# Kernel tuning notes

Measured on AMD Instinct MI355X. Metric: run time of the kernel, lower is better.

Reference implementation:

```python
import jax, jax.numpy as jnp
from jax import lax
import numpy as np

D_MODEL = 6      # problemDim
ED = 48          # d_inner = expand_factor * d_model = hidden_size
N = 32           # d_state
DCONV = 16       # d_conv
NLAYERS = 2
DT_RANK = 1      # ceil(d_model / 16)
NCLS = 4
B, L = 16, 1024
EPS = 1e-5


def setup_inputs() -> dict:
    key = jax.random.key(0)
    ks = jax.random.split(key, 12)
    rn = lambda k, s, sc=0.1: (jax.random.normal(k, s, dtype=jnp.float32) * sc)
    return {
        "x": jax.random.normal(ks[0], (B, L, D_MODEL), dtype=jnp.float32),
        "in_proj_w": rn(ks[1], (NLAYERS, D_MODEL, 2 * ED)),
        "conv_w": rn(ks[2], (NLAYERS, ED, DCONV)),
        "conv_b": jnp.zeros((NLAYERS, ED), jnp.float32),
        "x_proj_w": rn(ks[3], (NLAYERS, ED, DT_RANK + 2 * N)),
        "dt_w": rn(ks[4], (NLAYERS, DT_RANK, ED), 1.0),
        "dt_b": rn(ks[5], (NLAYERS, ED), 0.5),
        # S4D-real init: A = -[1..N]
        "A_log": jnp.log(jnp.broadcast_to(jnp.arange(1, N + 1, dtype=jnp.float32), (NLAYERS, ED, N))),
        "D": jnp.ones((NLAYERS, ED), jnp.float32),
        "norm_w": jnp.ones((NLAYERS, D_MODEL), jnp.float32),
        "out_proj_w": rn(ks[6], (NLAYERS - 1, ED, D_MODEL)),
        "fc_w": rn(ks[7], (ED, ED)),
        "fc_b": jnp.zeros((ED,), jnp.float32),
        "cls_w": rn(ks[8], (ED, NCLS)),
        "cls_b": jnp.zeros((NCLS,), jnp.float32),
        "reg_w": rn(ks[9], (ED, 1)),
        "reg_b": jnp.zeros((1,), jnp.float32),
    }


def rmsnorm(h, w):
    return h * lax.rsqrt(jnp.mean(h * h, axis=-1, keepdims=True) + EPS) * w


def dwconv_causal(xs, w, b):
    # xs: (B,L,ED), w: (ED,DCONV), b: (ED,) -> causal depthwise conv, output length L
    u = jnp.pad(xs.transpose(0, 2, 1), ((0, 0), (0, 0), (DCONV - 1, 0)))  # (B,ED,L+DCONV-1)
    out = lax.conv_general_dilated(u, w[:, None, :], window_strides=(1,), padding="VALID",
                                   feature_group_count=ED,
                                   dimension_numbers=("NCH", "OIH", "NCH"))  # (B,ED,L)
    return (out + b[None, :, None]).transpose(0, 2, 1)


def selective_scan(deltaA, deltaBx, Cm):
    # deltaA, deltaBx: (B,L,ED,N); Cm: (B,L,N) -> y: (B,L,ED)
    dA = deltaA.transpose(1, 0, 2, 3)
    dBx = deltaBx.transpose(1, 0, 2, 3)
    Ct = Cm.transpose(1, 0, 2)

    def step(h, inp):
        dA_t, dBx_t, C_t = inp
        h = dA_t * h + dBx_t                       # (B,ED,N)
        y = jnp.einsum("ben,bn->be", h, C_t)       # (B,ED)
        return h, y

    h0 = jnp.zeros(dA.shape[1:], dA.dtype)
    _, ys = lax.scan(step, h0, (dA, dBx, Ct))
    return ys.transpose(1, 0, 2)


def mamba_forward(x, in_proj_w, conv_w, conv_b, x_proj_w, dt_w, dt_b, A_log, D,
                  norm_w, out_proj_w, fc_w, fc_b, cls_w, cls_b, reg_w, reg_b):
    h = x
    for i in range(NLAYERS):
        res = h
        u = rmsnorm(h, norm_w[i])
        xz = u @ in_proj_w[i]                      # (B,L,2*ED)
        xs, z = jnp.split(xz, 2, axis=-1)
        xs = jax.nn.silu(dwconv_causal(xs, conv_w[i], conv_b[i]))
        dbc = xs @ x_proj_w[i]                     # (B,L,DT_RANK+2N)
        dlt = dbc[..., :DT_RANK]
        Bm = dbc[..., DT_RANK:DT_RANK + N]
        Cm = dbc[..., DT_RANK + N:]
        delta = jax.nn.softplus(dlt @ dt_w[i] + dt_b[i])   # (B,L,ED)
        A = -jnp.exp(A_log[i])                     # (ED,N)
        deltaA = jnp.exp(delta[..., None] * A)     # (B,L,ED,N)
        deltaBx = delta[..., None] * Bm[:, :, None, :] * xs[..., None]
        y = selective_scan(deltaA, deltaBx, Cm) + D[i] * xs
        y = y * jax.nn.silu(z)
        if i < NLAYERS - 1:
            h = y @ out_proj_w[i] + res
        else:
            h = y  # classifer=True: last block exposes d_inner (=hidden_size) features
    feat = jax.nn.relu(h[:, -1, :] @ fc_w + fc_b)  # (B,ED)
    class_logits = feat @ cls_w + cls_b            # (B,NCLS)
    mass_pred = (feat @ reg_w + reg_b)[..., 0]     # (B,)
    return class_logits, mass_pred


def reference(x, in_proj_w, conv_w, conv_b, x_proj_w, dt_w, dt_b, A_log, D,
              norm_w, out_proj_w, fc_w, fc_b, cls_w, cls_b, reg_w, reg_b):
    return mamba_forward(x, in_proj_w, conv_w, conv_b, x_proj_w, dt_w, dt_b, A_log, D,
                         norm_w, out_proj_w, fc_w, fc_b, cls_w, cls_b, reg_w, reg_b)
```

## Files before the change

### kernel.cpp

```cpp
#include <hip/hip_runtime.h>
#include <math.h>

#define BB 16
#define LL 1024
#define DM 6
#define ED 48
#define NST 32
#define DCONVK 16
#define NCLS 4
#define CH 32
#define HALO 15
#define NCF 16
#define CSF 64

__device__ __forceinline__ float softplus_f(float x) {
    return fmaxf(x, 0.f) + log1pf(expf(-fabsf(x)));
}
__device__ __forceinline__ float silu_f(float x) {
    return x / (1.f + __expf(-x));
}

template<int MODE>
__global__ __launch_bounds__(256) void pre_kernel(
    const float* __restrict__ hin,
    const float* __restrict__ ygT_in,
    const float* __restrict__ opw,
    const float* __restrict__ ipw,
    const float* __restrict__ nw,
    const float* __restrict__ cw,
    const float* __restrict__ cb,
    const float* __restrict__ xpw,
    const float* __restrict__ dtw,
    const float* __restrict__ dtb,
    float* __restrict__ xT,
    float* __restrict__ zT,
    float* __restrict__ dT,
    float* __restrict__ Bi,
    float* __restrict__ Ci)
{
    __shared__ float s_ipw[6*96];
    __shared__ float s_nw[6];
    __shared__ float s_cw[48*DCONVK];
    __shared__ float s_cb[48];
    __shared__ float s_xpw[48*65];
    __shared__ float s_dtw[48];
    __shared__ float s_dtb[48];
    __shared__ float s_opw[48*6];
    __shared__ float s_pp[(CH+HALO)*4*6];
    __shared__ float s_u[(CH+HALO)*7];
    __shared__ float s_raw[(CH+HALO)*49];
    __shared__ float s_xsT[48*CH];
    __shared__ float s_bc[64*33];
    __shared__ float s_dlt[CH];

    const int tid = threadIdx.x;
    const int b  = blockIdx.x >> 5;
    const int l0 = (blockIdx.x & 31) * CH;
    const int ROWS = CH + HALO;

    for (int i = tid; i < 6*96; i += 256) s_ipw[i] = ipw[i];
    if (tid < 6) s_nw[tid] = nw[tid];
    for (int i = tid; i < 48*DCONVK; i += 256) s_cw[i] = cw[i];
    if (tid < 48) s_cb[tid] = cb[tid];
    for (int i = tid; i < 48*65; i += 256) s_xpw[i] = xpw[i];
    if (tid < 48) { s_dtw[tid] = dtw[tid]; s_dtb[tid] = dtb[tid]; }
    if (MODE == 1) for (int i = tid; i < 48*6; i += 256) s_opw[i] = opw[i];
    __syncthreads();

    if (MODE == 0) {
        if (tid < ROWS) {
            int l = l0 - HALO + tid;
            float u[DM];
            if (l >= 0) {
                float ss = 0.f;
                const float* hp = hin + ((size_t)b*LL + l)*DM;
                #pragma unroll
                for (int d = 0; d < DM; ++d) { u[d] = hp[d]; ss += u[d]*u[d]; }
                float sc = rsqrtf(ss * (1.f/DM) + 1e-5f);
                #pragma unroll
                for (int d = 0; d < DM; ++d) u[d] *= sc * s_nw[d];
            } else {
                #pragma unroll
                for (int d = 0; d < DM; ++d) u[d] = 0.f;
            }
            #pragma unroll
            for (int d = 0; d < DM; ++d) s_u[tid*7+d] = u[d];
        }
        __syncthreads();
    } else {
        const int g = tid >> 6, t = tid & 63;
        if (t < ROWS) {
            int l = l0 - HALO + t;
            float pacc[DM] = {0,0,0,0,0,0};
            if (l >= 0) {
                for (int e = g*12; e < g*12 + 12; ++e) {
                    float v = ygT_in[((size_t)b*48 + e)*LL + l];
                    #pragma unroll
                    for (int d = 0; d < DM; ++d) pacc[d] += v * s_opw[e*DM+d];
                }
            }
            #pragma unroll
            for (int d = 0; d < DM; ++d) s_pp[(t*4+g)*DM+d] = pacc[d];
        }
        __syncthreads();
        if (tid < ROWS) {
            int l = l0 - HALO + tid;
            float u[DM];
            if (l >= 0) {
                const float* xr = hin + ((size_t)b*LL + l)*DM;
                float ss = 0.f;
                #pragma unroll
                for (int d = 0; d < DM; ++d) {
                    float hv = s_pp[(tid*4+0)*DM+d] + s_pp[(tid*4+1)*DM+d]
                             + s_pp[(tid*4+2)*DM+d] + s_pp[(tid*4+3)*DM+d] + xr[d];
                    u[d] = hv; ss += hv*hv;
                }
                float sc = rsqrtf(ss * (1.f/DM) + 1e-5f);
                #pragma unroll
                for (int d = 0; d < DM; ++d) u[d] *= sc * s_nw[d];
            } else {
                #pragma unroll
                for (int d = 0; d < DM; ++d) u[d] = 0.f;
            }
            #pragma unroll
            for (int d = 0; d < DM; ++d) s_u[tid*7+d] = u[d];
        }
        __syncthreads();
    }

    for (int i = tid; i < 96*ROWS; i += 256) {
        int j = i / ROWS, t = i - j*ROWS;
        float acc = 0.f;
        #pragma unroll
        for (int d = 0; d < DM; ++d) acc += s_u[t*7+d]*s_ipw[d*96+j];
        if (j < 48) s_raw[t*49+j] = acc;
        else if (t >= HALO)
            zT[((size_t)b*48 + (j-48))*LL + (l0 - HALO + t)] = silu_f(acc);
    }
    __syncthreads();

    for (int o = tid; o < 48*CH; o += 256) {
        int c = o >> 5, p = o & 31;
        float acc = s_cb[c];
        #pragma unroll
        for (int k = 0; k < DCONVK; ++k)
            acc += s_raw[(p+k)*49 + c] * s_cw[c*DCONVK + k];
        float v = silu_f(acc);
        s_xsT[c*CH + p] = v;
        xT[((size_t)b*48 + c)*LL + l0 + p] = v;
    }
    __syncthreads();

    {
        const int j = tid >> 3, g = tid & 7;
        float a0=0,a1=0,a2=0,a3=0;
        float c0=0,c1=0,c2=0,c3=0;
        for (int e = 0; e < 48; ++e) {
            float4 xv = *(const float4*)&s_xsT[e*CH + 4*g];
            float w1 = s_xpw[e*65 + 1 + j];
            float w2 = s_xpw[e*65 + 33 + j];
            a0 = fmaf(xv.x, w1, a0); a1 = fmaf(xv.y, w1, a1);
            a2 = fmaf(xv.z, w1, a2); a3 = fmaf(xv.w, w1, a3);
            c0 = fmaf(xv.x, w2, c0); c1 = fmaf(xv.y, w2, c1);
            c2 = fmaf(xv.z, w2, c2); c3 = fmaf(xv.w, w2, c3);
        }
        s_bc[j*33 + 4*g+0] = a0; s_bc[j*33 + 4*g+1] = a1;
        s_bc[j*33 + 4*g+2] = a2; s_bc[j*33 + 4*g+3] = a3;
        s_bc[(32+j)*33 + 4*g+0] = c0; s_bc[(32+j)*33 + 4*g+1] = c1;
        s_bc[(32+j)*33 + 4*g+2] = c2; s_bc[(32+j)*33 + 4*g+3] = c3;
    }
    if (tid < 32) {
        float acc = 0.f;
        for (int e = 0; e < 48; ++e) acc += s_xsT[e*CH + tid]*s_xpw[e*65];
        s_dlt[tid] = acc;
    }
    __syncthreads();

    for (int o = tid; o < 2*CH*32; o += 256) {
        int which = o >> 10;
        int l = (o >> 5) & (CH-1), n = o & 31;
        float v = s_bc[(which*32 + n)*33 + l];
        float* dst = which ? Ci : Bi;
        dst[((size_t)b*LL + l0 + l)*32 + n] = v;
    }

    for (int o = tid; o < 48*CH; o += 256) {
        int e = o >> 5, p = o & 31;
        float xv = s_dlt[p]*s_dtw[e] + s_dtb[e];
        dT[((size_t)b*48 + e)*LL + l0 + p] = softplus_f(xv);
    }
}

__global__ __launch_bounds__(1024) void scan_fused(
    const float* __restrict__ dT,
    const float* __restrict__ xT,
    const float* __restrict__ zT,
    const float* __restrict__ Bi,
    const float* __restrict__ Ci,
    const float* __restrict__ A_log,
    const float* __restrict__ Dw,
    float* __restrict__ ygT)
{
    __shared__ float2 sPH[2][NCF][32];
    __shared__ float2 sACa[2][NCF][32];
    __shared__ float  sYL[2][NCF][CSF];
    __shared__ float  sS [2][NCF][CSF];

    const int tid = threadIdx.x;
    const int c = tid >> 6;
    const int lane = tid & 63;
    const int eh = lane >> 5, n = lane & 31;
    const int b = blockIdx.x / 24;
    const int epair = blockIdx.x % 24;
    const int e = epair*2 + eh;

    const float Ac = -__expf(A_log[e*NST + n]);
    const float Dc = Dw[e];

    const size_t eb = ((size_t)b*48 + e)*LL + c*CSF;
    const float4* dp = (const float4*)(dT + eb);
    const float4* xp = (const float4*)(xT + eb);
    const float*  bp = Bi + ((size_t)b*LL + c*CSF)*32 + n;
    const float*  cp = Ci + ((size_t)b*LL + c*CSF)*32 + n;

    float h = 0.f, S = 0.f;

    #pragma unroll
    for (int q = 0; q < CSF/4; ++q) {
        float4 d4 = dp[q], x4 = xp[q];
        float b0 = bp[(4*q+0)*32], b1 = bp[(4*q+1)*32];
        float b2 = bp[(4*q+2)*32], b3 = bp[(4*q+3)*32];
        float c0 = cp[(4*q+0)*32], c1 = cp[(4*q+1)*32];
        float c2 = cp[(4*q+2)*32], c3 = cp[(4*q+3)*32];
        float p0, p1, p2, p3;
        h = fmaf(__expf(d4.x*Ac), h, d4.x*x4.x*b0); p0 = h*c0;
        h = fmaf(__expf(d4.y*Ac), h, d4.y*x4.y*b1); p1 = h*c1;
        h = fmaf(__expf(d4.z*Ac), h, d4.z*x4.z*b2); p2 = h*c2;
        h = fmaf(__expf(d4.w*Ac), h, d4.w*x4.w*b3); p3 = h*c3;
        float s0 = S + d4.x, s1 = s0 + d4.y, s2 = s1 + d4.z, s3 = s2 + d4.w;
        S = s3;
        if (n == 0) *(float4*)&sS[eh][c][4*q] = make_float4(s0, s1, s2, s3);
        float q0 = p0 + __shfl_xor(p0, 16);
        float q1 = p1 + __shfl_xor(p1, 16);
        float q2 = p2 + __shfl_xor(p2, 16);
        float q3 = p3 + __shfl_xor(p3, 16);
        float m01 = (n & 16) ? q1 : q0;
        float m23 = (n & 16) ? q3 : q2;
        m01 += __shfl_xor(m01, 8);
        m23 += __shfl_xor(m23, 8);
        float mm = (n & 8) ? m23 : m01;
        mm += __shfl_xor(mm, 4);
        mm += __shfl_xor(mm, 2);
        mm += __shfl_xor(mm, 1);
        if ((n & 7) == 0) {
            int vidx = ((n >> 4) & 1) | (((n >> 3) & 1) << 1);
            float xv = (vidx & 2) ? ((vidx & 1) ? x4.w : x4.z)
                                  : ((vidx & 1) ? x4.y : x4.x);
            sYL[eh][c][4*q + vidx] = fmaf(Dc, xv, mm);
        }
    }
    sPH[eh][c][n] = make_float2(__expf(Ac*S), h);
    __syncthreads();

    if (tid < 64) {
        float2 v[NCF];
        #pragma unroll
        for (int k = 0; k < NCF; ++k) v[k] = sPH[eh][k][n];
        float acc = 0.f;
        #pragma unroll
        for (int k = 0; k < NCF; ++k) {
            sACa[eh][k][n] = make_float2(Ac, acc);
            acc = fmaf(v[k].x, acc, v[k].y);
        }
    }
    __syncthreads();

    {
        const int t = lane;
        const float4* cpt = (const float4*)(Ci + ((size_t)b*LL + c*CSF + t)*32);
        float4 Cv[8];
        #pragma unroll
        for (int k = 0; k < 8; ++k) Cv[k] = cpt[k];

        #pragma unroll
        for (int eh2 = 0; eh2 < 2; ++eh2) {
            const int e2 = epair*2 + eh2;
            const float St = sS[eh2][c][t];
            const float yl = sYL[eh2][c][t];
            float corr = 0.f;
            #pragma unroll
            for (int k = 0; k < 8; ++k) {
                float4 cv = Cv[k];
                float4 w0 = *(const float4*)&sACa[eh2][c][4*k];
                float4 w1 = *(const float4*)&sACa[eh2][c][4*k+2];
                corr = fmaf(cv.x * __expf(w0.x*St), w0.y, corr);
                corr = fmaf(cv.y * __expf(w0.z*St), w0.w, corr);
                corr = fmaf(cv.z * __expf(w1.x*St), w1.y, corr);
                corr = fmaf(cv.w * __expf(w1.z*St), w1.w, corr);
            }
            const size_t o = ((size_t)b*48 + e2)*LL + c*CSF + t;
            ygT[o] = (yl + corr) * zT[o];
        }
    }
}

__global__ __launch_bounds__(1024) void head_kernel(
    const float* __restrict__ ygT,
    const float* __restrict__ fcw, const float* __restrict__ fcb,
    const float* __restrict__ clw, const float* __restrict__ clb,
    const float* __restrict__ rgw, const float* __restrict__ rgb,
    float* __restrict__ out)
{
    __shared__ float s_h[BB*48];
    __shared__ float s_f[BB*48];
    const int tid = threadIdx.x;
    const int b = tid >> 6, j = tid & 63;
    if (j < 48) s_h[b*48+j] = ygT[((size_t)b*48 + j)*LL + (LL-1)];
    __syncthreads();
    if (j < 48) {
        float acc = fcb[j];
        for (int k = 0; k < 48; ++k) acc += s_h[b*48+k]*fcw[k*48+j];
        s_f[b*48+j] = fmaxf(acc, 0.f);
    }
    __syncthreads();
    if (j < NCLS) {
        float acc = clb[j];
        for (int k = 0; k < 48; ++k) acc += s_f[b*48+k]*clw[k*NCLS+j];
        out[b*NCLS + j] = acc;
    }
    if (j == NCLS) {
        float acc = rgb[0];
        for (int k = 0; k < 48; ++k) acc += s_f[b*48+k]*rgw[k];
        out[BB*NCLS + b] = acc;
    }
}

extern "C" void kernel_launch(void* const* d_in, const int* in_sizes, int n_in,
                              void* d_out, int out_size, void* d_ws, size_t ws_size,
                              hipStream_t stream)
{
    const float* x     = (const float*)d_in[0];
    const float* ipw   = (const float*)d_in[1];
    const float* cw    = (const float*)d_in[2];
    const float* cb    = (const float*)d_in[3];
    const float* xpw   = (const float*)d_in[4];
    const float* dtw   = (const float*)d_in[5];
    const float* dtb   = (const float*)d_in[6];
    const float* A_log = (const float*)d_in[7];
    const float* Dw    = (const float*)d_in[8];
    const float* nw    = (const float*)d_in[9];
    const float* opw   = (const float*)d_in[10];
    const float* fcw   = (const float*)d_in[11];
    const float* fcb   = (const float*)d_in[12];
    const float* clw   = (const float*)d_in[13];
    const float* clb   = (const float*)d_in[14];
    const float* rgw   = (const float*)d_in[15];
    const float* rgb   = (const float*)d_in[16];
    float* out = (float*)d_out;

    float* ws = (float*)d_ws;
    const size_t BL = (size_t)BB*LL;
    float* xT  = ws;
    float* zT  = xT  + BL*48;
    float* dT  = zT  + BL*48;
    float* Bi  = dT  + BL*48;
    float* Ci  = Bi  + BL*32;
    float* ygT = Ci  + BL*32;

    const dim3 preGrid(BB*32), preBlk(256);
    const dim3 scanGrid(BB*24), scanBlk(1024);

    pre_kernel<0><<<preGrid, preBlk, 0, stream>>>(
        x, nullptr, nullptr, ipw, nw, cw, cb, xpw, dtw, dtb,
        xT, zT, dT, Bi, Ci);
    scan_fused<<<scanGrid, scanBlk, 0, stream>>>(
        dT, xT, zT, Bi, Ci, A_log, Dw, ygT);

    pre_kernel<1><<<preGrid, preBlk, 0, stream>>>(
        x, ygT, opw, ipw + 6*96, nw + 6, cw + 48*DCONVK, cb + 48,
        xpw + 48*65, dtw + 48, dtb + 48,
        xT, zT, dT, Bi, Ci);
    scan_fused<<<scanGrid, scanBlk, 0, stream>>>(
        dT, xT, zT, Bi, Ci, A_log + 48*NST, Dw + 48, ygT);

    head_kernel<<<dim3(1), dim3(1024), 0, stream>>>(
        ygT, fcw, fcb, clw, clb, rgw, rgb, out);
}
```

Measured before the change: 201.0 us.

## Halve pre-kernel chunk size and split scan blocks to one channel each

```diff
diff --git a/kernel.cpp b/kernel.cpp
--- a/kernel.cpp
+++ b/kernel.cpp
@@ -8,10 +8,10 @@
 #define NST 32
 #define DCONVK 16
 #define NCLS 4
-#define CH 32
+#define CH 16
 #define HALO 15
-#define NCF 16
-#define CSF 64
+#define SNC 16
+#define SCS 64
 
 __device__ __forceinline__ float softplus_f(float x) {
     return fmaxf(x, 0.f) + log1pf(expf(-fabsf(x)));
@@ -21,7 +21,7 @@
 }
 
 template<int MODE>
-__global__ __launch_bounds__(256) void pre_kernel(
+__global__ __launch_bounds__(256, 4) void pre_kernel(
     const float* __restrict__ hin,
     const float* __restrict__ ygT_in,
     const float* __restrict__ opw,
@@ -50,12 +50,12 @@
     __shared__ float s_u[(CH+HALO)*7];
     __shared__ float s_raw[(CH+HALO)*49];
     __shared__ float s_xsT[48*CH];
-    __shared__ float s_bc[64*33];
+    __shared__ float s_bc[64*(CH+1)];
     __shared__ float s_dlt[CH];
 
     const int tid = threadIdx.x;
-    const int b  = blockIdx.x >> 5;
-    const int l0 = (blockIdx.x & 31) * CH;
+    const int b  = blockIdx.x >> 6;
+    const int l0 = (blockIdx.x & 63) * CH;
     const int ROWS = CH + HALO;
 
     for (int i = tid; i < 6*96; i += 256) s_ipw[i] = ipw[i];
@@ -140,7 +140,7 @@
     __syncthreads();
 
     for (int o = tid; o < 48*CH; o += 256) {
-        int c = o >> 5, p = o & 31;
+        int c = o >> 4, p = o & 15;
         float acc = s_cb[c];
         #pragma unroll
         for (int k = 0; k < DCONVK; ++k)
@@ -152,24 +152,18 @@
     __syncthreads();
 
     {
-        const int j = tid >> 3, g = tid & 7;
+        const int j = tid >> 2, g = tid & 3;
         float a0=0,a1=0,a2=0,a3=0;
-        float c0=0,c1=0,c2=0,c3=0;
         for (int e = 0; e < 48; ++e) {
             float4 xv = *(const float4*)&s_xsT[e*CH + 4*g];
-            float w1 = s_xpw[e*65 + 1 + j];
-            float w2 = s_xpw[e*65 + 33 + j];
-            a0 = fmaf(xv.x, w1, a0); a1 = fmaf(xv.y, w1, a1);
-            a2 = fmaf(xv.z, w1, a2); a3 = fmaf(xv.w, w1, a3);
-            c0 = fmaf(xv.x, w2, c0); c1 = fmaf(xv.y, w2, c1);
-            c2 = fmaf(xv.z, w2, c2); c3 = fmaf(xv.w, w2, c3);
-        }
-        s_bc[j*33 + 4*g+0] = a0; s_bc[j*33 + 4*g+1] = a1;
-        s_bc[j*33 + 4*g+2] = a2; s_bc[j*33 + 4*g+3] = a3;
-        s_bc[(32+j)*33 + 4*g+0] = c0; s_bc[(32+j)*33 + 4*g+1] = c1;
-        s_bc[(32+j)*33 + 4*g+2] = c2; s_bc[(32+j)*33 + 4*g+3] = c3;
-    }
-    if (tid < 32) {
+            float w = s_xpw[e*65 + 1 + j];
+            a0 = fmaf(xv.x, w, a0); a1 = fmaf(xv.y, w, a1);
+            a2 = fmaf(xv.z, w, a2); a3 = fmaf(xv.w, w, a3);
+        }
+        s_bc[j*(CH+1) + 4*g+0] = a0; s_bc[j*(CH+1) + 4*g+1] = a1;
+        s_bc[j*(CH+1) + 4*g+2] = a2; s_bc[j*(CH+1) + 4*g+3] = a3;
+    }
+    if (tid < CH) {
         float acc = 0.f;
         for (int e = 0; e < 48; ++e) acc += s_xsT[e*CH + tid]*s_xpw[e*65];
         s_dlt[tid] = acc;
@@ -177,21 +171,21 @@
     __syncthreads();
 
     for (int o = tid; o < 2*CH*32; o += 256) {
-        int which = o >> 10;
+        int which = o >> 9;
         int l = (o >> 5) & (CH-1), n = o & 31;
-        float v = s_bc[(which*32 + n)*33 + l];
+        float v = s_bc[(which*32 + n)*(CH+1) + l];
         float* dst = which ? Ci : Bi;
         dst[((size_t)b*LL + l0 + l)*32 + n] = v;
     }
 
     for (int o = tid; o < 48*CH; o += 256) {
-        int e = o >> 5, p = o & 31;
+        int e = o >> 4, p = o & 15;
         float xv = s_dlt[p]*s_dtw[e] + s_dtb[e];
         dT[((size_t)b*48 + e)*LL + l0 + p] = softplus_f(xv);
     }
 }
 
-__global__ __launch_bounds__(1024) void scan_fused(
+__global__ __launch_bounds__(512, 6) void scan_fused(
     const float* __restrict__ dT,
     const float* __restrict__ xT,
     const float* __restrict__ zT,
@@ -201,32 +195,31 @@
     const float* __restrict__ Dw,
     float* __restrict__ ygT)
 {
-    __shared__ float2 sPH[2][NCF][32];
-    __shared__ float2 sACa[2][NCF][32];
-    __shared__ float  sYL[2][NCF][CSF];
-    __shared__ float  sS [2][NCF][CSF];
+    __shared__ float2 sPH[SNC][32];
+    __shared__ float2 sACa[SNC][32];
+    __shared__ float  sYL[SNC][SCS];
+    __shared__ float  sS [SNC][SCS];
 
     const int tid = threadIdx.x;
-    const int c = tid >> 6;
     const int lane = tid & 63;
-    const int eh = lane >> 5, n = lane & 31;
-    const int b = blockIdx.x / 24;
-    const int epair = blockIdx.x % 24;
-    const int e = epair*2 + eh;
+    const int ch = lane >> 5, n = lane & 31;
+    const int c = (tid >> 6)*2 + ch;
+    const int b = blockIdx.x / 48;
+    const int e = blockIdx.x % 48;
 
     const float Ac = -__expf(A_log[e*NST + n]);
     const float Dc = Dw[e];
 
-    const size_t eb = ((size_t)b*48 + e)*LL + c*CSF;
+    const size_t eb = ((size_t)b*48 + e)*LL + c*SCS;
     const float4* dp = (const float4*)(dT + eb);
     const float4* xp = (const float4*)(xT + eb);
-    const float*  bp = Bi + ((size_t)b*LL + c*CSF)*32 + n;
-    const float*  cp = Ci + ((size_t)b*LL + c*CSF)*32 + n;
+    const float*  bp = Bi + ((size_t)b*LL + c*SCS)*32 + n;
+    const float*  cp = Ci + ((size_t)b*LL + c*SCS)*32 + n;
 
     float h = 0.f, S = 0.f;
 
     #pragma unroll
-    for (int q = 0; q < CSF/4; ++q) {
+    for (int q = 0; q < SCS/4; ++q) {
         float4 d4 = dp[q], x4 = xp[q];
         float b0 = bp[(4*q+0)*32], b1 = bp[(4*q+1)*32];
         float b2 = bp[(4*q+2)*32], b3 = bp[(4*q+3)*32];
@@ -239,7 +232,7 @@
         h = fmaf(__expf(d4.w*Ac), h, d4.w*x4.w*b3); p3 = h*c3;
         float s0 = S + d4.x, s1 = s0 + d4.y, s2 = s1 + d4.z, s3 = s2 + d4.w;
         S = s3;
-        if (n == 0) *(float4*)&sS[eh][c][4*q] = make_float4(s0, s1, s2, s3);
+        if (n == 0) *(float4*)&sS[c][4*q] = make_float4(s0, s1, s2, s3);
         float q0 = p0 + __shfl_xor(p0, 16);
         float q1 = p1 + __shfl_xor(p1, 16);
         float q2 = p2 + __shfl_xor(p2, 16);
@@ -256,51 +249,45 @@
             int vidx = ((n >> 4) & 1) | (((n >> 3) & 1) << 1);
             float xv = (vidx & 2) ? ((vidx & 1) ? x4.w : x4.z)
                                   : ((vidx & 1) ? x4.y : x4.x);
-            sYL[eh][c][4*q + vidx] = fmaf(Dc, xv, mm);
-        }
-    }
-    sPH[eh][c][n] = make_float2(__expf(Ac*S), h);
-    __syncthreads();
-
-    if (tid < 64) {
-        float2 v[NCF];
-        #pragma unroll
-        for (int k = 0; k < NCF; ++k) v[k] = sPH[eh][k][n];
+            sYL[c][4*q + vidx] = fmaf(Dc, xv, mm);
+        }
+    }
+    sPH[c][n] = make_float2(__expf(Ac*S), h);
+    __syncthreads();
+
+    if (tid < 32) {
+        float2 v[SNC];
+        #pragma unroll
+        for (int k = 0; k < SNC; ++k) v[k] = sPH[k][tid];
         float acc = 0.f;
         #pragma unroll
-        for (int k = 0; k < NCF; ++k) {
-            sACa[eh][k][n] = make_float2(Ac, acc);
+        for (int k = 0; k < SNC; ++k) {
+            sACa[k][tid] = make_float2(Ac, acc);
             acc = fmaf(v[k].x, acc, v[k].y);
         }
     }
     __syncthreads();
 
-    {
+    #pragma unroll
+    for (int r = 0; r < 2; ++r) {
+        const int c2 = (tid >> 6) + 8*r;
         const int t = lane;
-        const float4* cpt = (const float4*)(Ci + ((size_t)b*LL + c*CSF + t)*32);
-        float4 Cv[8];
-        #pragma unroll
-        for (int k = 0; k < 8; ++k) Cv[k] = cpt[k];
-
-        #pragma unroll
-        for (int eh2 = 0; eh2 < 2; ++eh2) {
-            const int e2 = epair*2 + eh2;
-            const float St = sS[eh2][c][t];
-            const float yl = sYL[eh2][c][t];
-            float corr = 0.f;
-            #pragma unroll
-            for (int k = 0; k < 8; ++k) {
-                float4 cv = Cv[k];
-                float4 w0 = *(const float4*)&sACa[eh2][c][4*k];
-                float4 w1 = *(const float4*)&sACa[eh2][c][4*k+2];
-                corr = fmaf(cv.x * __expf(w0.x*St), w0.y, corr);
-                corr = fmaf(cv.y * __expf(w0.z*St), w0.w, corr);
-                corr = fmaf(cv.z * __expf(w1.x*St), w1.y, corr);
-                corr = fmaf(cv.w * __expf(w1.z*St), w1.w, corr);
-            }
-            const size_t o = ((size_t)b*48 + e2)*LL + c*CSF + t;
-            ygT[o] = (yl + corr) * zT[o];
-        }
+        const float St = sS[c2][t];
+        const float yl = sYL[c2][t];
+        const float4* cpt = (const float4*)(Ci + ((size_t)b*LL + c2*SCS + t)*32);
+        float corr = 0.f;
+        #pragma unroll
+        for (int k = 0; k < 8; ++k) {
+            float4 cv = cpt[k];
+            float4 w0 = *(const float4*)&sACa[c2][4*k];
+            float4 w1 = *(const float4*)&sACa[c2][4*k+2];
+            corr = fmaf(cv.x * __expf(w0.x*St), w0.y, corr);
+            corr = fmaf(cv.y * __expf(w0.z*St), w0.w, corr);
+            corr = fmaf(cv.z * __expf(w1.x*St), w1.y, corr);
+            corr = fmaf(cv.w * __expf(w1.z*St), w1.w, corr);
+        }
+        const size_t o = ((size_t)b*48 + e)*LL + c2*SCS + t;
+        ygT[o] = (yl + corr) * zT[o];
     }
 }
 
@@ -367,8 +354,8 @@
     float* Ci  = Bi  + BL*32;
     float* ygT = Ci  + BL*32;
 
-    const dim3 preGrid(BB*32), preBlk(256);
-    const dim3 scanGrid(BB*24), scanBlk(1024);
+    const dim3 preGrid(BB*64), preBlk(256);
+    const dim3 scanGrid(BB*48), scanBlk(512);
 
     pre_kernel<0><<<preGrid, preBlk, 0, stream>>>(
         x, nullptr, nullptr, ipw, nw, cw, cb, xpw, dtw, dtb,
```

Measured after the change: 194.4 us. -3.3%, faster.
